# Performance work log

Hardware: AMD Instinct MI355X
Metric: run time of the kernel (lower is better)

## Reference

```python
import jax, jax.numpy as jnp
import numpy as np

N_NODES = 50000
N_EDGES = 1600000
IN_DIM = 128
HIDDEN = 16
HEADS = 8
OUT_DIM = 64


def setup_inputs() -> dict:
    key = jax.random.key(0)
    k1, k2, k3, k4, k5 = jax.random.split(key, 5)
    h = jax.random.normal(k1, (N_NODES, IN_DIM), dtype=jnp.float32)
    W1 = jax.random.normal(k2, (IN_DIM, HEADS * HIDDEN), dtype=jnp.float32) * (IN_DIM ** -0.5)
    W2 = jax.random.normal(k3, (HEADS * HIDDEN, OUT_DIM), dtype=jnp.float32) * ((HEADS * HIDDEN) ** -0.5)
    src = jax.random.randint(k4, (N_EDGES,), 0, N_NODES, dtype=jnp.int32)
    dst = jax.random.randint(k5, (N_EDGES,), 0, N_NODES, dtype=jnp.int32)
    return {"h": h, "W1": W1, "W2": W2, "src": src, "dst": dst}


def dot_gat_conv(h, W, src, dst, num_heads, out_feats):
    # Project and split heads: [N, H, D]
    feat = (h @ W).reshape(-1, num_heads, out_feats)
    fs = feat[src]                       # [E, H, D] gather
    fd = feat[dst]                       # [E, H, D] gather
    scale = jnp.asarray(out_feats, feat.dtype) ** -0.5
    e = jnp.einsum('ehd,ehd->eh', fs, fd) * scale  # [E, H] scaled dot score
    # Edge softmax over incoming edges of each destination node
    m = jax.ops.segment_max(e, dst, num_segments=N_NODES)   # [N, H]
    m = jnp.where(jnp.isfinite(m), m, jnp.zeros_like(m))    # isolated nodes
    ex = jnp.exp(e - m[dst])                                 # [E, H]
    denom = jax.ops.segment_sum(ex, dst, num_segments=N_NODES)  # [N, H]
    a = ex / jnp.maximum(denom[dst], jnp.asarray(1e-9, ex.dtype))  # [E, H]
    # Weighted scatter-sum aggregation: [N, H, D]
    return jax.ops.segment_sum(a[:, :, None] * fs, dst, num_segments=N_NODES)


def reference(h, W1, W2, src, dst):
    h1 = dot_gat_conv(h, W1, src, dst, HEADS, HIDDEN)  # [N, H, hidden]
    h1 = jax.nn.elu(h1).reshape(N_NODES, HEADS * HIDDEN)  # flatten(1)
    # Dropout: eval-mode identity
    h2 = dot_gat_conv(h1, W2, src, dst, 1, OUT_DIM)  # [N, 1, out]
    return h2.mean(axis=1)  # [N, out]
```

## Files before the change

### kernel.cpp

```cpp
#include <hip/hip_runtime.h>
#include <hip/hip_bf16.h>

#define N_NODES 50000
#define N_EDGES 1600000
#define NBUCK 98
#define EPB 4096
#define NB_A ((N_EDGES + EPB - 1) / EPB)

typedef short bf16x8 __attribute__((ext_vector_type(8)));
typedef float f32x4  __attribute__((ext_vector_type(4)));
typedef float f32x2  __attribute__((ext_vector_type(2)));

#if __has_builtin(__builtin_amdgcn_exp2f)
#define EXP2(x) __builtin_amdgcn_exp2f(x)
#else
#define EXP2(x) exp2f(x)
#endif
#define LOG2E 1.44269504088896340736f

__device__ __forceinline__ float bf16_raw_to_f32(unsigned short u) {
    return __uint_as_float(((unsigned)u) << 16);
}
__device__ __forceinline__ unsigned short f32_to_bf16_raw(float v) {
    unsigned u = __float_as_uint(v);
    return (unsigned short)((u + 0x7fffu + ((u >> 16) & 1u)) >> 16);
}
__device__ __forceinline__ float load_elem(const void* p, size_t i, int f) {
    if (f) return ((const float*)p)[i];
    return bf16_raw_to_f32(((const unsigned short*)p)[i]);
}
__device__ __forceinline__ void unpack8v(uint4 u, f32x2* f) {
    f[0] = (f32x2){__uint_as_float(u.x << 16), __uint_as_float(u.x & 0xffff0000u)};
    f[1] = (f32x2){__uint_as_float(u.y << 16), __uint_as_float(u.y & 0xffff0000u)};
    f[2] = (f32x2){__uint_as_float(u.z << 16), __uint_as_float(u.z & 0xffff0000u)};
    f[3] = (f32x2){__uint_as_float(u.w << 16), __uint_as_float(u.w & 0xffff0000u)};
}

__global__ void detect_dtype_kernel(const unsigned short* __restrict__ w1raw,
                                    int* __restrict__ flag, int* __restrict__ bcnt) {
    __shared__ float red[256];
    if (threadIdx.x < NBUCK) bcnt[threadIdx.x] = 0;
    float mx = 0.f;
    for (int i = threadIdx.x * 2; i < 16384; i += 512) {
        float v = fabsf(bf16_raw_to_f32(w1raw[i]));
        if (!isnan(v)) mx = fmaxf(mx, v);
    }
    red[threadIdx.x] = mx;
    __syncthreads();
    for (int s = 128; s > 0; s >>= 1) {
        if (threadIdx.x < s) red[threadIdx.x] = fmaxf(red[threadIdx.x], red[threadIdx.x + s]);
        __syncthreads();
    }
    if (threadIdx.x == 0) flag[0] = (red[0] > 1e4f) ? 1 : 0;
}

#define WPAD 136
__global__ void prep_kernel(const void* __restrict__ W1, const void* __restrict__ W2,
                            unsigned short* __restrict__ W1T,
                            unsigned short* __restrict__ W2T,
                            const int* __restrict__ flag) {
    const int f = *flag;
    int bid = blockIdx.x, tid = threadIdx.x;
    if (bid < 8) {
        int n = bid * 16 + (tid & 15);
        int kb = (tid >> 4) * 8;
        for (int j = 0; j < 8; ++j)
            W1T[n * WPAD + kb + j] = f32_to_bf16_raw(load_elem(W1, (size_t)(kb + j) * 128 + n, f));
    } else {
        int n = (bid - 8) * 16 + (tid & 15);
        int kb = (tid >> 4) * 8;
        for (int j = 0; j < 8; ++j)
            W2T[n * WPAD + kb + j] = f32_to_bf16_raw(load_elem(W2, (size_t)(kb + j) * 64 + n, f));
    }
}

__global__ void bucket_count_kernel(const int* __restrict__ dst,
                                    int* __restrict__ bcnt, int E) {
    __shared__ int hist[NBUCK];
    int t = threadIdx.x;
    if (t < NBUCK) hist[t] = 0;
    __syncthreads();
    int e0 = blockIdx.x * EPB;
    for (int k = 0; k < 16; ++k) {
        int e = e0 + k * 256 + t;
        if (e < E) atomicAdd(&hist[dst[e] >> 9], 1);
    }
    __syncthreads();
    if (t < NBUCK && hist[t]) atomicAdd(&bcnt[t], hist[t]);
}

__global__ void bucket_scan_kernel(const int* __restrict__ bcnt,
                                   int* __restrict__ bbase, int* __restrict__ bcur) {
    __shared__ int tmp[128];
    int t = threadIdx.x;
    int v = (t < NBUCK) ? bcnt[t] : 0;
    tmp[t] = v;
    __syncthreads();
    for (int off = 1; off < 128; off <<= 1) {
        int x = (t >= off) ? tmp[t - off] : 0;
        __syncthreads();
        tmp[t] += x;
        __syncthreads();
    }
    if (t < NBUCK) { int ex = tmp[t] - v; bbase[t] = ex; bcur[t] = ex; }
    if (t == NBUCK - 1) bbase[NBUCK] = tmp[t];
}

__global__ void binA_kernel(const int* __restrict__ src, const int* __restrict__ dst,
                            int* __restrict__ bcur, unsigned* __restrict__ inter, int E) {
    __shared__ int hist[NBUCK], gbase[NBUCK], cur[NBUCK];
    int t = threadIdx.x;
    if (t < NBUCK) hist[t] = 0;
    __syncthreads();
    int e0 = blockIdx.x * EPB;
    for (int k = 0; k < 16; ++k) {
        int e = e0 + k * 256 + t;
        if (e < E) atomicAdd(&hist[dst[e] >> 9], 1);
    }
    __syncthreads();
    if (t < NBUCK) {
        int hv = hist[t];
        gbase[t] = hv ? atomicAdd(&bcur[t], hv) : 0;
        cur[t] = 0;
    }
    __syncthreads();
    for (int k = 0; k < 16; ++k) {
        int e = e0 + k * 256 + t;
        if (e < E) {
            int d = dst[e];
            int b = d >> 9;
            int off = atomicAdd(&cur[b], 1);
            inter[gbase[b] + off] = (unsigned)src[e] | ((unsigned)(d & 511) << 16);
        }
    }
}

__global__ void binB_kernel(const unsigned* __restrict__ inter,
                            const int* __restrict__ bbase,
                            int* __restrict__ csr_src, int* __restrict__ start,
                            int N, int E) {
    int b = blockIdx.x;
    int node0 = b << 9;
    int lo = bbase[b], hi = bbase[b + 1];
    __shared__ int hist[512];
    __shared__ int t2[256];
    int t = threadIdx.x;
    hist[t] = 0; hist[t + 256] = 0;
    __syncthreads();
    for (int e = lo + t; e < hi; e += 256) atomicAdd(&hist[inter[e] >> 16], 1);
    __syncthreads();
    int s0 = hist[2 * t], s1 = hist[2 * t + 1];
    t2[t] = s0 + s1;
    __syncthreads();
    for (int off = 1; off < 256; off <<= 1) {
        int x = (t >= off) ? t2[t - off] : 0;
        __syncthreads();
        t2[t] += x;
        __syncthreads();
    }
    int base = (t == 0) ? 0 : t2[t - 1];
    hist[2 * t] = base;
    hist[2 * t + 1] = base + s0;
    __syncthreads();
    int nodeCnt = min(512, N - node0);
    for (int i = t; i < nodeCnt; i += 256) start[node0 + i] = lo + hist[i];
    if (b == NBUCK - 1 && t == 0) start[N] = E;
    __syncthreads();
    for (int e = lo + t; e < hi; e += 256) {
        unsigned u = inter[e];
        int slot = lo + atomicAdd(&hist[u >> 16], 1);
        csr_src[slot] = (int)(u & 0xffffu);
    }
}

__global__ void gemm1_mfma_kernel(const void* __restrict__ h,
                                  const unsigned short* __restrict__ W1T,
                                  unsigned short* __restrict__ feat1, int N,
                                  const int* __restrict__ flag) {
    const int f = *flag;
    int lane = threadIdx.x & 63;
    int rbase = blockIdx.x * 64 + (threadIdx.x >> 6) * 16;
    int arow = rbase + (lane & 15);
    int arowc = min(arow, N - 1);
    int kb0 = (lane >> 4) * 8;

    f32x4 acc[8];
#pragma unroll
    for (int t = 0; t < 8; ++t) acc[t] = (f32x4){0.f, 0.f, 0.f, 0.f};

#pragma unroll
    for (int ks = 0; ks < 4; ++ks) {
        int kb = ks * 32 + kb0;
        bf16x8 afrag;
        if (f == 0) {
            afrag = *(const bf16x8*)((const unsigned short*)h + (size_t)arowc * 128 + kb);
        } else {
            const float* hp = (const float*)h + (size_t)arowc * 128 + kb;
#pragma unroll
            for (int j = 0; j < 8; ++j) afrag[j] = (short)f32_to_bf16_raw(hp[j]);
        }
#pragma unroll
        for (int t = 0; t < 8; ++t) {
            int n = t * 16 + (lane & 15);
            bf16x8 bfrag = *(const bf16x8*)(W1T + n * WPAD + kb);
            acc[t] = __builtin_amdgcn_mfma_f32_16x16x32_bf16(afrag, bfrag, acc[t], 0, 0, 0);
        }
    }
    int orow0 = rbase + (lane >> 4) * 4;
    int col = lane & 15;
#pragma unroll
    for (int t = 0; t < 8; ++t)
#pragma unroll
        for (int r = 0; r < 4; ++r) {
            int row = orow0 + r;
            if (row < N)
                feat1[(size_t)row * 128 + t * 16 + col] = f32_to_bf16_raw(acc[t][r]);
        }
}

__global__ void gemm2_mfma_kernel(const unsigned short* __restrict__ agg1e,
                                  const unsigned short* __restrict__ W2T,
                                  unsigned short* __restrict__ feat2, int N) {
    int lane = threadIdx.x & 63;
    int rbase = blockIdx.x * 64 + (threadIdx.x >> 6) * 16;
    int arow = rbase + (lane & 15);
    int arowc = min(arow, N - 1);
    int kb0 = (lane >> 4) * 8;

    f32x4 acc[4];
#pragma unroll
    for (int t = 0; t < 4; ++t) acc[t] = (f32x4){0.f, 0.f, 0.f, 0.f};

#pragma unroll
    for (int ks = 0; ks < 4; ++ks) {
        int kb = ks * 32 + kb0;
        bf16x8 afrag = *(const bf16x8*)(agg1e + (size_t)arowc * 128 + kb);
#pragma unroll
        for (int t = 0; t < 4; ++t) {
            int n = t * 16 + (lane & 15);
            bf16x8 bfrag = *(const bf16x8*)(W2T + n * WPAD + kb);
            acc[t] = __builtin_amdgcn_mfma_f32_16x16x32_bf16(afrag, bfrag, acc[t], 0, 0, 0);
        }
    }
    int orow0 = rbase + (lane >> 4) * 4;
    int col = lane & 15;
#pragma unroll
    for (int t = 0; t < 4; ++t)
#pragma unroll
        for (int r = 0; r < 4; ++r) {
            int row = orow0 + r;
            if (row < N)
                feat2[(size_t)row * 64 + t * 16 + col] = f32_to_bf16_raw(acc[t][r]);
        }
}

#define GAT1_PROC(U0, U1)                                                     \
    {                                                                         \
        f32x2 f0[4], f1[4];                                                   \
        unpack8v(U0, f0); unpack8v(U1, f1);                                   \
        f32x2 p0 = fd2[0] * f0[0];                                            \
        f32x2 p1 = fd2[0] * f1[0];                                            \
        _Pragma("unroll")                                                     \
        for (int k = 1; k < 4; ++k) { p0 += fd2[k] * f0[k]; p1 += fd2[k] * f1[k]; } \
        float q0 = p0.x + p0.y, q1 = p1.x + p1.y;                             \
        q0 += __shfl_xor(q0, 1); q1 += __shfl_xor(q1, 1);                     \
        float w0 = EXP2(q0), w1 = EXP2(q1);                                   \
        f32x2 W0 = (f32x2){w0, w0}, W1 = (f32x2){w1, w1};                     \
        _Pragma("unroll")                                                     \
        for (int k = 0; k < 4; ++k) { acc2[k] += W0 * f0[k]; acc2[k] += W1 * f1[k]; } \
        l += w0 + w1;                                                         \
    }

__global__ void gat1_kernel(const unsigned short* __restrict__ feat1,
                            const int* __restrict__ csr_src,
                            const int* __restrict__ start,
                            unsigned short* __restrict__ agg1e, int N) {
    int wave = blockIdx.x * 4 + (threadIdx.x >> 6);
    if (wave >= N) return;
    int lane = threadIdx.x & 63;
    int grp = lane >> 4, gl = lane & 15;
    const char* fb = (const char*)feat1;
    unsigned loff = (unsigned)gl << 4;
    f32x2 fd2[4];
    unpack8v(*(const uint4*)(fb + (((unsigned)wave << 8) + loff)), fd2);
    const float SC = 0.25f * LOG2E;
    const f32x2 SC2 = (f32x2){SC, SC};
#pragma unroll
    for (int k = 0; k < 4; ++k) fd2[k] *= SC2;

    float l = 0.f;
    f32x2 acc2[4];
#pragma unroll
    for (int k = 0; k < 4; ++k) acc2[k] = (f32x2){0.f, 0.f};

    int e0 = start[wave], e1 = start[wave + 1];
    int nfull = (e1 - e0) >> 3;
    int base = e0;
    uint4 u0, u1;
    if (nfull > 0) {
        int s0 = csr_src[base + grp];
        int s1 = csr_src[base + 4 + grp];
        u0 = *(const uint4*)(fb + (((unsigned)s0 << 8) + loff));
        u1 = *(const uint4*)(fb + (((unsigned)s1 << 8) + loff));
    }
    for (int it = 0; it < nfull - 1; ++it) {
        int nb = base + 8;
        int s0 = csr_src[nb + grp];
        int s1 = csr_src[nb + 4 + grp];
        uint4 n0 = *(const uint4*)(fb + (((unsigned)s0 << 8) + loff));
        uint4 n1 = *(const uint4*)(fb + (((unsigned)s1 << 8) + loff));
        GAT1_PROC(u0, u1);
        u0 = n0; u1 = n1; base = nb;
    }
    if (nfull > 0) { GAT1_PROC(u0, u1); base += 8; }
    for (; base < e1; base += 4) {
        int ed = base + grp;
        bool act = ed < e1;
        int s = act ? csr_src[ed] : 0;
        uint4 u = *(const uint4*)(fb + (((unsigned)s << 8) + loff));
        f32x2 fv[4]; unpack8v(u, fv);
        f32x2 p = fd2[0] * fv[0];
#pragma unroll
        for (int k = 1; k < 4; ++k) p += fd2[k] * fv[k];
        float q = p.x + p.y;
        q += __shfl_xor(q, 1);
        float w = act ? EXP2(q) : 0.f;
        f32x2 W = (f32x2){w, w};
#pragma unroll
        for (int k = 0; k < 4; ++k) acc2[k] += W * fv[k];
        l += w;
    }
#pragma unroll
    for (int off = 16; off <= 32; off <<= 1) {
        l += __shfl_xor(l, off);
#pragma unroll
        for (int k = 0; k < 4; ++k) {
            acc2[k].x += __shfl_xor(acc2[k].x, off);
            acc2[k].y += __shfl_xor(acc2[k].y, off);
        }
    }
    if (grp == 0) {
        float rcp = 1.f / fmaxf(l, 1e-9f);
        float v[8];
#pragma unroll
        for (int k = 0; k < 4; ++k) {
            float x0 = acc2[k].x * rcp;
            float x1 = acc2[k].y * rcp;
            v[2 * k]     = (x0 > 0.f) ? x0 : expm1f(x0);
            v[2 * k + 1] = (x1 > 0.f) ? x1 : expm1f(x1);
        }
        uint4 pk;
        pk.x = (unsigned)f32_to_bf16_raw(v[0]) | ((unsigned)f32_to_bf16_raw(v[1]) << 16);
        pk.y = (unsigned)f32_to_bf16_raw(v[2]) | ((unsigned)f32_to_bf16_raw(v[3]) << 16);
        pk.z = (unsigned)f32_to_bf16_raw(v[4]) | ((unsigned)f32_to_bf16_raw(v[5]) << 16);
        pk.w = (unsigned)f32_to_bf16_raw(v[6]) | ((unsigned)f32_to_bf16_raw(v[7]) << 16);
        *(uint4*)(agg1e + (size_t)wave * 128 + gl * 8) = pk;
    }
}

#define GAT2_PROC(U0, U1)                                                     \
    {                                                                         \
        f32x2 f0[4], f1[4];                                                   \
        unpack8v(U0, f0); unpack8v(U1, f1);                                   \
        f32x2 p0 = fd2[0] * f0[0];                                            \
        f32x2 p1 = fd2[0] * f1[0];                                            \
        _Pragma("unroll")                                                     \
        for (int k = 1; k < 4; ++k) { p0 += fd2[k] * f0[k]; p1 += fd2[k] * f1[k]; } \
        float q0 = p0.x + p0.y, q1 = p1.x + p1.y;                             \
        q0 += __shfl_xor(q0, 1); q1 += __shfl_xor(q1, 1);                     \
        q0 += __shfl_xor(q0, 2); q1 += __shfl_xor(q1, 2);                     \
        q0 += __shfl_xor(q0, 4); q1 += __shfl_xor(q1, 4);                     \
        float w0 = EXP2(q0), w1 = EXP2(q1);                                   \
        f32x2 W0 = (f32x2){w0, w0}, W1 = (f32x2){w1, w1};                     \
        _Pragma("unroll")                                                     \
        for (int k = 0; k < 4; ++k) { acc2[k] += W0 * f0[k]; acc2[k] += W1 * f1[k]; } \
        l += w0 + w1;                                                         \
    }

__global__ void gat2_kernel(const unsigned short* __restrict__ feat2,
                            const int* __restrict__ csr_src,
                            const int* __restrict__ start,
                            void* __restrict__ out, int N,
                            const int* __restrict__ flag) {
    int wave = blockIdx.x * 4 + (threadIdx.x >> 6);
    if (wave >= N) return;
    int lane = threadIdx.x & 63;
    int grp = lane >> 3, gl = lane & 7;
    const int f = *flag;
    const char* fb = (const char*)feat2;
    unsigned loff = (unsigned)gl << 4;
    f32x2 fd2[4];
    unpack8v(*(const uint4*)(fb + (((unsigned)wave << 7) + loff)), fd2);
    const float SC = 0.125f * LOG2E;
    const f32x2 SC2 = (f32x2){SC, SC};
#pragma unroll
    for (int k = 0; k < 4; ++k) fd2[k] *= SC2;

    float l = 0.f;
    f32x2 acc2[4];
#pragma unroll
    for (int k = 0; k < 4; ++k) acc2[k] = (f32x2){0.f, 0.f};

    int e0 = start[wave], e1 = start[wave + 1];
    int nfull = (e1 - e0) >> 4;
    int base = e0;
    uint4 u0, u1;
    if (nfull > 0) {
        int s0 = csr_src[base + grp];
        int s1 = csr_src[base + 8 + grp];
        u0 = *(const uint4*)(fb + (((unsigned)s0 << 7) + loff));
        u1 = *(const uint4*)(fb + (((unsigned)s1 << 7) + loff));
    }
    for (int it = 0; it < nfull - 1; ++it) {
        int nb = base + 16;
        int s0 = csr_src[nb + grp];
        int s1 = csr_src[nb + 8 + grp];
        uint4 n0 = *(const uint4*)(fb + (((unsigned)s0 << 7) + loff));
        uint4 n1 = *(const uint4*)(fb + (((unsigned)s1 << 7) + loff));
        GAT2_PROC(u0, u1);
        u0 = n0; u1 = n1; base = nb;
    }
    if (nfull > 0) { GAT2_PROC(u0, u1); base += 16; }
    for (; base < e1; base += 8) {
        int ed = base + grp;
        bool act = ed < e1;
        int s = act ? csr_src[ed] : 0;
        uint4 u = *(const uint4*)(fb + (((unsigned)s << 7) + loff));
        f32x2 fv[4]; unpack8v(u, fv);
        f32x2 p = fd2[0] * fv[0];
#pragma unroll
        for (int k = 1; k < 4; ++k) p += fd2[k] * fv[k];
        float q = p.x + p.y;
        q += __shfl_xor(q, 1);
        q += __shfl_xor(q, 2);
        q += __shfl_xor(q, 4);
        float w = act ? EXP2(q) : 0.f;
        f32x2 W = (f32x2){w, w};
#pragma unroll
        for (int k = 0; k < 4; ++k) acc2[k] += W * fv[k];
        l += w;
    }
#pragma unroll
    for (int off = 8; off <= 32; off <<= 1) {
        l += __shfl_xor(l, off);
#pragma unroll
        for (int k = 0; k < 4; ++k) {
            acc2[k].x += __shfl_xor(acc2[k].x, off);
            acc2[k].y += __shfl_xor(acc2[k].y, off);
        }
    }
    if (grp == 0) {
        float rcp = 1.f / fmaxf(l, 1e-9f);
        float v[8];
#pragma unroll
        for (int k = 0; k < 4; ++k) {
            v[2 * k]     = acc2[k].x * rcp;
            v[2 * k + 1] = acc2[k].y * rcp;
        }
        if (f) {
            float* op = (float*)out + (size_t)wave * 64 + gl * 8;
            *(float4*)(op)     = (float4){v[0], v[1], v[2], v[3]};
            *(float4*)(op + 4) = (float4){v[4], v[5], v[6], v[7]};
        } else {
            uint4 pk;
            pk.x = (unsigned)f32_to_bf16_raw(v[0]) | ((unsigned)f32_to_bf16_raw(v[1]) << 16);
            pk.y = (unsigned)f32_to_bf16_raw(v[2]) | ((unsigned)f32_to_bf16_raw(v[3]) << 16);
            pk.z = (unsigned)f32_to_bf16_raw(v[4]) | ((unsigned)f32_to_bf16_raw(v[5]) << 16);
            pk.w = (unsigned)f32_to_bf16_raw(v[6]) | ((unsigned)f32_to_bf16_raw(v[7]) << 16);
            *(uint4*)((unsigned short*)out + (size_t)wave * 64 + gl * 8) = pk;
        }
    }
}

extern "C" void kernel_launch(void* const* d_in, const int* in_sizes, int n_in,
                              void* d_out, int out_size, void* d_ws, size_t ws_size,
                              hipStream_t stream) {
    const void* h  = d_in[0];
    const void* W1 = d_in[1];
    const void* W2 = d_in[2];
    const int* src = (const int*)d_in[3];
    const int* dst = (const int*)d_in[4];

    float* ws = (float*)d_ws;
    unsigned short* feat1 = (unsigned short*)ws;
    unsigned short* agg1e = (unsigned short*)(ws + 3200000);
    unsigned short* feat2 = (unsigned short*)ws;
    unsigned* inter       = (unsigned*)(ws + 6400000);
    int*   csr_src        = (int*)(ws + 9600000);
    int*   start          = (int*)(ws + 11200000);
    int*   flag           = (int*)(ws + 11330000);
    int*   bcnt           = (int*)(ws + 11331000);
    int*   bbase          = (int*)(ws + 11332000);
    int*   bcur           = (int*)(ws + 11333000);
    unsigned short* W1T   = (unsigned short*)(ws + 11340000);
    unsigned short* W2T   = (unsigned short*)(ws + 11350000);

    detect_dtype_kernel<<<1, 256, 0, stream>>>((const unsigned short*)W1, flag, bcnt);
    prep_kernel<<<12, 256, 0, stream>>>(W1, W2, W1T, W2T, flag);

    bucket_count_kernel<<<NB_A, 256, 0, stream>>>(dst, bcnt, N_EDGES);
    bucket_scan_kernel<<<1, 128, 0, stream>>>(bcnt, bbase, bcur);
    binA_kernel<<<NB_A, 256, 0, stream>>>(src, dst, bcur, inter, N_EDGES);
    binB_kernel<<<NBUCK, 256, 0, stream>>>(inter, bbase, csr_src, start, N_NODES, N_EDGES);

    gemm1_mfma_kernel<<<(N_NODES + 63) / 64, 256, 0, stream>>>(h, W1T, feat1, N_NODES, flag);
    gat1_kernel<<<(N_NODES + 3) / 4, 256, 0, stream>>>(feat1, csr_src, start, agg1e, N_NODES);
    gemm2_mfma_kernel<<<(N_NODES + 63) / 64, 256, 0, stream>>>(agg1e, W2T, feat2, N_NODES);
    gat2_kernel<<<(N_NODES + 3) / 4, 256, 0, stream>>>(feat2, csr_src, start, d_out, N_NODES, flag);
}
```

Baseline: 285.1 us.

## Fuse CSR build stages with weight prep and split GEMM1 across binning kernels

```diff
diff --git a/kernel.cpp b/kernel.cpp
--- a/kernel.cpp
+++ b/kernel.cpp
@@ -3,9 +3,11 @@
 
 #define N_NODES 50000
 #define N_EDGES 1600000
-#define NBUCK 98
 #define EPB 4096
 #define NB_A ((N_EDGES + EPB - 1) / EPB)
+#define NBUCK2 391
+#define BSHIFT 7
+#define BMASK 127
 
 typedef short bf16x8 __attribute__((ext_vector_type(8)));
 typedef float f32x4  __attribute__((ext_vector_type(4)));
@@ -36,150 +38,72 @@
     f[3] = (f32x2){__uint_as_float(u.w << 16), __uint_as_float(u.w & 0xffff0000u)};
 }
 
-__global__ void detect_dtype_kernel(const unsigned short* __restrict__ w1raw,
-                                    int* __restrict__ flag, int* __restrict__ bcnt) {
+__device__ __forceinline__ int block_detect(const unsigned short* w1raw) {
     __shared__ float red[256];
-    if (threadIdx.x < NBUCK) bcnt[threadIdx.x] = 0;
+    int t = threadIdx.x;
     float mx = 0.f;
-    for (int i = threadIdx.x * 2; i < 16384; i += 512) {
+    for (int i = t * 2; i < 16384; i += 512) {
         float v = fabsf(bf16_raw_to_f32(w1raw[i]));
         if (!isnan(v)) mx = fmaxf(mx, v);
     }
-    red[threadIdx.x] = mx;
+    red[t] = mx;
     __syncthreads();
     for (int s = 128; s > 0; s >>= 1) {
-        if (threadIdx.x < s) red[threadIdx.x] = fmaxf(red[threadIdx.x], red[threadIdx.x + s]);
-        __syncthreads();
-    }
-    if (threadIdx.x == 0) flag[0] = (red[0] > 1e4f) ? 1 : 0;
+        if (t < s) red[t] = fmaxf(red[t], red[t + s]);
+        __syncthreads();
+    }
+    return (red[0] > 1e4f) ? 1 : 0;
 }
 
 #define WPAD 136
-__global__ void prep_kernel(const void* __restrict__ W1, const void* __restrict__ W2,
-                            unsigned short* __restrict__ W1T,
-                            unsigned short* __restrict__ W2T,
-                            const int* __restrict__ flag) {
-    const int f = *flag;
-    int bid = blockIdx.x, tid = threadIdx.x;
-    if (bid < 8) {
-        int n = bid * 16 + (tid & 15);
-        int kb = (tid >> 4) * 8;
-        for (int j = 0; j < 8; ++j)
-            W1T[n * WPAD + kb + j] = f32_to_bf16_raw(load_elem(W1, (size_t)(kb + j) * 128 + n, f));
+
+__global__ void k1_count_prep_kernel(const int* __restrict__ dst, int E,
+                                     int* __restrict__ bcnt,
+                                     const void* __restrict__ W1,
+                                     const void* __restrict__ W2,
+                                     unsigned short* __restrict__ W1T,
+                                     unsigned short* __restrict__ W2T,
+                                     int* __restrict__ flag) {
+    int bid = blockIdx.x;
+    if (bid < NB_A) {
+        __shared__ int hist[NBUCK2];
+        int t = threadIdx.x;
+        for (int i = t; i < NBUCK2; i += 256) hist[i] = 0;
+        __syncthreads();
+        int e0 = bid * EPB;
+        for (int k = 0; k < 16; ++k) {
+            int e = e0 + k * 256 + t;
+            if (e < E) atomicAdd(&hist[dst[e] >> BSHIFT], 1);
+        }
+        __syncthreads();
+        for (int i = t; i < NBUCK2; i += 256)
+            if (hist[i]) atomicAdd(&bcnt[i], hist[i]);
+    } else if (bid < NB_A + 12) {
+        const int f = block_detect((const unsigned short*)W1);
+        int b2 = bid - NB_A, tid = threadIdx.x;
+        if (b2 < 8) {
+            int n = b2 * 16 + (tid & 15);
+            int kb = (tid >> 4) * 8;
+            for (int j = 0; j < 8; ++j)
+                W1T[n * WPAD + kb + j] = f32_to_bf16_raw(load_elem(W1, (size_t)(kb + j) * 128 + n, f));
+        } else {
+            int n = (b2 - 8) * 16 + (tid & 15);
+            int kb = (tid >> 4) * 8;
+            for (int j = 0; j < 8; ++j)
+                W2T[n * WPAD + kb + j] = f32_to_bf16_raw(load_elem(W2, (size_t)(kb + j) * 64 + n, f));
+        }
     } else {
-        int n = (bid - 8) * 16 + (tid & 15);
-        int kb = (tid >> 4) * 8;
-        for (int j = 0; j < 8; ++j)
-            W2T[n * WPAD + kb + j] = f32_to_bf16_raw(load_elem(W2, (size_t)(kb + j) * 64 + n, f));
-    }
-}
-
-__global__ void bucket_count_kernel(const int* __restrict__ dst,
-                                    int* __restrict__ bcnt, int E) {
-    __shared__ int hist[NBUCK];
-    int t = threadIdx.x;
-    if (t < NBUCK) hist[t] = 0;
-    __syncthreads();
-    int e0 = blockIdx.x * EPB;
-    for (int k = 0; k < 16; ++k) {
-        int e = e0 + k * 256 + t;
-        if (e < E) atomicAdd(&hist[dst[e] >> 9], 1);
-    }
-    __syncthreads();
-    if (t < NBUCK && hist[t]) atomicAdd(&bcnt[t], hist[t]);
-}
-
-__global__ void bucket_scan_kernel(const int* __restrict__ bcnt,
-                                   int* __restrict__ bbase, int* __restrict__ bcur) {
-    __shared__ int tmp[128];
-    int t = threadIdx.x;
-    int v = (t < NBUCK) ? bcnt[t] : 0;
-    tmp[t] = v;
-    __syncthreads();
-    for (int off = 1; off < 128; off <<= 1) {
-        int x = (t >= off) ? tmp[t - off] : 0;
-        __syncthreads();
-        tmp[t] += x;
-        __syncthreads();
-    }
-    if (t < NBUCK) { int ex = tmp[t] - v; bbase[t] = ex; bcur[t] = ex; }
-    if (t == NBUCK - 1) bbase[NBUCK] = tmp[t];
-}
-
-__global__ void binA_kernel(const int* __restrict__ src, const int* __restrict__ dst,
-                            int* __restrict__ bcur, unsigned* __restrict__ inter, int E) {
-    __shared__ int hist[NBUCK], gbase[NBUCK], cur[NBUCK];
-    int t = threadIdx.x;
-    if (t < NBUCK) hist[t] = 0;
-    __syncthreads();
-    int e0 = blockIdx.x * EPB;
-    for (int k = 0; k < 16; ++k) {
-        int e = e0 + k * 256 + t;
-        if (e < E) atomicAdd(&hist[dst[e] >> 9], 1);
-    }
-    __syncthreads();
-    if (t < NBUCK) {
-        int hv = hist[t];
-        gbase[t] = hv ? atomicAdd(&bcur[t], hv) : 0;
-        cur[t] = 0;
-    }
-    __syncthreads();
-    for (int k = 0; k < 16; ++k) {
-        int e = e0 + k * 256 + t;
-        if (e < E) {
-            int d = dst[e];
-            int b = d >> 9;
-            int off = atomicAdd(&cur[b], 1);
-            inter[gbase[b] + off] = (unsigned)src[e] | ((unsigned)(d & 511) << 16);
-        }
-    }
-}
-
-__global__ void binB_kernel(const unsigned* __restrict__ inter,
-                            const int* __restrict__ bbase,
-                            int* __restrict__ csr_src, int* __restrict__ start,
-                            int N, int E) {
-    int b = blockIdx.x;
-    int node0 = b << 9;
-    int lo = bbase[b], hi = bbase[b + 1];
-    __shared__ int hist[512];
-    __shared__ int t2[256];
-    int t = threadIdx.x;
-    hist[t] = 0; hist[t + 256] = 0;
-    __syncthreads();
-    for (int e = lo + t; e < hi; e += 256) atomicAdd(&hist[inter[e] >> 16], 1);
-    __syncthreads();
-    int s0 = hist[2 * t], s1 = hist[2 * t + 1];
-    t2[t] = s0 + s1;
-    __syncthreads();
-    for (int off = 1; off < 256; off <<= 1) {
-        int x = (t >= off) ? t2[t - off] : 0;
-        __syncthreads();
-        t2[t] += x;
-        __syncthreads();
-    }
-    int base = (t == 0) ? 0 : t2[t - 1];
-    hist[2 * t] = base;
-    hist[2 * t + 1] = base + s0;
-    __syncthreads();
-    int nodeCnt = min(512, N - node0);
-    for (int i = t; i < nodeCnt; i += 256) start[node0 + i] = lo + hist[i];
-    if (b == NBUCK - 1 && t == 0) start[N] = E;
-    __syncthreads();
-    for (int e = lo + t; e < hi; e += 256) {
-        unsigned u = inter[e];
-        int slot = lo + atomicAdd(&hist[u >> 16], 1);
-        csr_src[slot] = (int)(u & 0xffffu);
-    }
-}
-
-__global__ void gemm1_mfma_kernel(const void* __restrict__ h,
-                                  const unsigned short* __restrict__ W1T,
-                                  unsigned short* __restrict__ feat1, int N,
-                                  const int* __restrict__ flag) {
-    const int f = *flag;
+        int f = block_detect((const unsigned short*)W1);
+        if (threadIdx.x == 0) flag[0] = f;
+    }
+}
+
+__device__ __forceinline__ void gemm1_body(const void* __restrict__ h,
+                                           const unsigned short* __restrict__ W1T,
+                                           unsigned short* __restrict__ feat1, int N,
+                                           int f, int blk, int row_base) {
     int lane = threadIdx.x & 63;
-    int rbase = blockIdx.x * 64 + (threadIdx.x >> 6) * 16;
+    int rbase = row_base + blk * 64 + (threadIdx.x >> 6) * 16;
     int arow = rbase + (lane & 15);
     int arowc = min(arow, N - 1);
     int kb0 = (lane >> 4) * 8;
@@ -216,6 +140,119 @@
             if (row < N)
                 feat1[(size_t)row * 128 + t * 16 + col] = f32_to_bf16_raw(acc[t][r]);
         }
+}
+
+#define G1LO 391
+#define G1OFF (G1LO * 64)
+
+__global__ void k2_binA_gemm1lo_kernel(const int* __restrict__ src,
+                                       const int* __restrict__ dst,
+                                       const int* __restrict__ bcnt,
+                                       int* __restrict__ bcur,
+                                       unsigned* __restrict__ inter, int E,
+                                       const void* __restrict__ h,
+                                       const unsigned short* __restrict__ W1T,
+                                       unsigned short* __restrict__ feat1, int N,
+                                       const int* __restrict__ flag) {
+    int bid = blockIdx.x;
+    if (bid >= NB_A) {
+        gemm1_body(h, W1T, feat1, N, *flag, bid - NB_A, 0);
+        return;
+    }
+    __shared__ int hist[NBUCK2], P[NBUCK2], cur[NBUCK2];
+    __shared__ int sc2[256];
+    int t = threadIdx.x;
+    for (int i = t; i < NBUCK2; i += 256) { hist[i] = 0; cur[i] = 0; }
+    __syncthreads();
+    int e0 = bid * EPB;
+    for (int k = 0; k < 16; ++k) {
+        int e = e0 + k * 256 + t;
+        if (e < E) atomicAdd(&hist[dst[e] >> BSHIFT], 1);
+    }
+    int i0 = 2 * t, i1 = 2 * t + 1;
+    int v0 = (i0 < NBUCK2) ? bcnt[i0] : 0;
+    int v1 = (i1 < NBUCK2) ? bcnt[i1] : 0;
+    sc2[t] = v0 + v1;
+    __syncthreads();
+    for (int off = 1; off < 256; off <<= 1) {
+        int x = (t >= off) ? sc2[t - off] : 0;
+        __syncthreads();
+        sc2[t] += x;
+        __syncthreads();
+    }
+    int exclp = sc2[t] - v0 - v1;
+    if (i0 < NBUCK2) P[i0] = exclp;
+    if (i1 < NBUCK2) P[i1] = exclp + v0;
+    __syncthreads();
+    for (int i = t; i < NBUCK2; i += 256) {
+        int hv = hist[i];
+        if (hv) P[i] += atomicAdd(&bcur[i], hv);
+    }
+    __syncthreads();
+    for (int k = 0; k < 16; ++k) {
+        int e = e0 + k * 256 + t;
+        if (e < E) {
+            int d = dst[e];
+            int b = d >> BSHIFT;
+            int off = atomicAdd(&cur[b], 1);
+            inter[P[b] + off] = (unsigned)src[e] | ((unsigned)(d & BMASK) << 16);
+        }
+    }
+}
+
+__global__ void k3_binB_gemm1hi_kernel(const unsigned* __restrict__ inter,
+                                       const int* __restrict__ bcnt,
+                                       int* __restrict__ csr_src,
+                                       int* __restrict__ start,
+                                       int N, int E,
+                                       const void* __restrict__ h,
+                                       const unsigned short* __restrict__ W1T,
+                                       unsigned short* __restrict__ feat1,
+                                       const int* __restrict__ flag) {
+    int bid = blockIdx.x;
+    if (bid >= NBUCK2) {
+        gemm1_body(h, W1T, feat1, N, *flag, bid - NBUCK2, G1OFF);
+        return;
+    }
+    int b = bid;
+    int node0 = b << BSHIFT;
+    __shared__ int red[256];
+    __shared__ int hist[128];
+    __shared__ int tmp[128];
+    int t = threadIdx.x;
+    int part = 0;
+    for (int i = t; i < b; i += 256) part += bcnt[i];
+    red[t] = part;
+    __syncthreads();
+    for (int s = 128; s > 0; s >>= 1) {
+        if (t < s) red[t] += red[t + s];
+        __syncthreads();
+    }
+    int lo = red[0];
+    int hi = lo + bcnt[b];
+    if (t < 128) hist[t] = 0;
+    __syncthreads();
+    for (int e = lo + t; e < hi; e += 256) atomicAdd(&hist[inter[e] >> 16], 1);
+    __syncthreads();
+    int own = (t < 128) ? hist[t] : 0;
+    if (t < 128) tmp[t] = own;
+    __syncthreads();
+    for (int off = 1; off < 128; off <<= 1) {
+        int x = (t >= off && t < 128) ? tmp[t - off] : 0;
+        __syncthreads();
+        if (t < 128) tmp[t] += x;
+        __syncthreads();
+    }
+    int nodeCnt = min(128, N - node0);
+    if (t < nodeCnt) start[node0 + t] = lo + (tmp[t] - own);
+    if (t < 128) hist[t] = lo + (tmp[t] - own);
+    if (b == NBUCK2 - 1 && t == 0) start[N] = E;
+    __syncthreads();
+    for (int e = lo + t; e < hi; e += 256) {
+        unsigned u = inter[e];
+        int slot = atomicAdd(&hist[u >> 16], 1);
+        csr_src[slot] = (int)(u & 0xffffu);
+    }
 }
 
 __global__ void gemm2_mfma_kernel(const unsigned short* __restrict__ agg1e,
@@ -490,20 +527,21 @@
     int*   start          = (int*)(ws + 11200000);
     int*   flag           = (int*)(ws + 11330000);
     int*   bcnt           = (int*)(ws + 11331000);
-    int*   bbase          = (int*)(ws + 11332000);
-    int*   bcur           = (int*)(ws + 11333000);
+    int*   bcur           = bcnt + NBUCK2;
     unsigned short* W1T   = (unsigned short*)(ws + 11340000);
     unsigned short* W2T   = (unsigned short*)(ws + 11350000);
 
-    detect_dtype_kernel<<<1, 256, 0, stream>>>((const unsigned short*)W1, flag, bcnt);
-    prep_kernel<<<12, 256, 0, stream>>>(W1, W2, W1T, W2T, flag);
-
-    bucket_count_kernel<<<NB_A, 256, 0, stream>>>(dst, bcnt, N_EDGES);
-    bucket_scan_kernel<<<1, 128, 0, stream>>>(bcnt, bbase, bcur);
-    binA_kernel<<<NB_A, 256, 0, stream>>>(src, dst, bcur, inter, N_EDGES);
-    binB_kernel<<<NBUCK, 256, 0, stream>>>(inter, bbase, csr_src, start, N_NODES, N_EDGES);
-
-    gemm1_mfma_kernel<<<(N_NODES + 63) / 64, 256, 0, stream>>>(h, W1T, feat1, N_NODES, flag);
+    hipMemsetAsync(bcnt, 0, 2 * NBUCK2 * sizeof(int), stream);
+
+    k1_count_prep_kernel<<<NB_A + 13, 256, 0, stream>>>(
+        dst, N_EDGES, bcnt, W1, W2, W1T, W2T, flag);
+
+    k2_binA_gemm1lo_kernel<<<NB_A + G1LO, 256, 0, stream>>>(
+        src, dst, bcnt, bcur, inter, N_EDGES, h, W1T, feat1, N_NODES, flag);
+
+    k3_binB_gemm1hi_kernel<<<NBUCK2 + G1LO, 256, 0, stream>>>(
+        inter, bcnt, csr_src, start, N_NODES, N_EDGES, h, W1T, feat1, flag);
+
     gat1_kernel<<<(N_NODES + 3) / 4, 256, 0, stream>>>(feat1, csr_src, start, agg1e, N_NODES);
     gemm2_mfma_kernel<<<(N_NODES + 63) / 64, 256, 0, stream>>>(agg1e, W2T, feat2, N_NODES);
     gat2_kernel<<<(N_NODES + 3) / 4, 256, 0, stream>>>(feat2, csr_src, start, d_out, N_NODES, flag);
```

Result: faster. 245.4 us (-13.9%).
